# Optimization experiments

Measured on AMD Instinct MI355X. Metric: run time of the kernel, lower is better.

## Reference

```python
import jax, jax.numpy as jnp
import numpy as np

B = 8192      # batch (num nodes)
D = 256       # embedding dim
K = 8         # positives per node -> nnz = B*K
EPS = 1e-8


def setup_inputs() -> dict:
    key = jax.random.key(0)
    k_emb, k_val = jax.random.split(key)
    embeddings = jax.random.normal(k_emb, (B, D), dtype=jnp.float32)
    # structured sparse positive mask: node i is positive with (i+1..i+K) mod B
    # -> unique pairs, row-major sorted (coalesced), no self loops
    rows = jnp.repeat(jnp.arange(B, dtype=jnp.int64), K)           # [B*K]
    offs = jnp.tile(jnp.arange(1, K + 1, dtype=jnp.int64), B)      # [B*K]
    cols = (rows + offs) % B
    pos_vals = jax.random.uniform(k_val, (B * K,), dtype=jnp.float32)
    temperature = jnp.float32(0.5)  # learnable scalar nn.Parameter
    return {
        "embeddings": embeddings,
        "pos_vals": pos_vals,
        "temperature": temperature,
        "pos_row": rows,
        "pos_col": cols,
    }


def reference(embeddings, pos_vals, temperature, pos_row, pos_col):
    n = embeddings.shape[0]
    # F.normalize(p=2, dim=1) with eps=1e-12
    norm = jnp.linalg.norm(embeddings, axis=1, keepdims=True)
    z = embeddings / jnp.maximum(norm, 1e-12)

    temp = jax.nn.softplus(temperature)
    sim = jnp.matmul(z, z.T) / temp                                 # [B,B]
    sim = sim - jax.lax.stop_gradient(jnp.max(sim, axis=1, keepdims=True))

    pos_dense = jnp.zeros((n, n), dtype=bool).at[pos_row, pos_col].set(True)
    identity = jnp.eye(n, dtype=bool)
    neg_mask = (~pos_dense) & (~identity)

    # pos weights: 'inverse_sim' -> 1 - values, min-max normalized
    pos_w = 1.0 - pos_vals
    pos_w = (pos_w - jnp.min(pos_w)) / (jnp.max(pos_w) - jnp.min(pos_w) + EPS)

    # neg weights: 'inverse_sim' -> min-max over negative sims, +1; weight_mat=1 elsewhere
    neg_min = jnp.min(jnp.where(neg_mask, sim, jnp.inf))
    neg_max = jnp.max(jnp.where(neg_mask, sim, -jnp.inf))
    neg_w = (sim - neg_min) / (neg_max - neg_min + EPS) + 1.0
    log_weight = jnp.where(neg_mask, jnp.log(neg_w), 0.0)

    log_probs = sim - jax.nn.logsumexp(sim + log_weight, axis=1, keepdims=True)

    pos_log = log_probs[pos_row, pos_col]   # same ordering as torch boolean index (coalesced mask)
    loss = -jnp.mean(pos_log * pos_w)
    return loss
```

## Files before the change

kernel.cpp:

```cpp
#include <hip/hip_runtime.h>

#define NB 8192
#define ND 256
#define NMASK 8191
#define CEPS 1e-8f
#define L2E 1.4426950408889634f
#define LN2 0.6931471805599453f
#define SC1 0x7F7F7F7F

#if __has_builtin(__builtin_amdgcn_exp2f)
#define EXP2(x) __builtin_amdgcn_exp2f(x)
#else
#define EXP2(x) exp2f(x)
#endif

#define DPPF(x, ctrl) \
  __int_as_float(__builtin_amdgcn_update_dpp(0, __float_as_int(x), (ctrl), 0xF, 0xF, true))

__device__ __forceinline__ float sum16(float x) {
  x += DPPF(x, 0xB1);
  x += DPPF(x, 0x4E);
  x += DPPF(x, 0x124);
  x += DPPF(x, 0x128);
  return x;
}
__device__ __forceinline__ float min16(float x) {
  x = fminf(x, DPPF(x, 0xB1));
  x = fminf(x, DPPF(x, 0x4E));
  x = fminf(x, DPPF(x, 0x124));
  x = fminf(x, DPPF(x, 0x128));
  return x;
}
__device__ __forceinline__ float max16(float x) {
  x = fmaxf(x, DPPF(x, 0xB1));
  x = fmaxf(x, DPPF(x, 0x4E));
  x = fmaxf(x, DPPF(x, 0x124));
  x = fmaxf(x, DPPF(x, 0x128));
  return x;
}

typedef float f32x4 __attribute__((ext_vector_type(4)));
typedef int v8i __attribute__((ext_vector_type(8)));
typedef int v4i __attribute__((ext_vector_type(4)));
union V8 { v8i v; v4i q[2]; };


__global__ void k_norm(const float* __restrict__ emb, const float* __restrict__ temperature,
                       const float* __restrict__ pos_vals, char* __restrict__ zb8,
                       float* __restrict__ bpvmin, float* __restrict__ bpvmax,
                       float* __restrict__ out) {
  const int tid = threadIdx.x, lane = tid & 63, w = tid >> 6;
  const int bid = blockIdx.x;
  if (bid == 0 && tid == 0) out[0] = 0.f;
  float sp = log1pf(expf(temperature[0]));
  float alpha = sqrtf(L2E / sp);
  int row = bid * 4 + w;
  const float4 e = *(const float4*)(emb + row * ND + lane * 4);
  float ss = e.x * e.x + e.y * e.y + e.z * e.z + e.w * e.w;
#pragma unroll
  for (int mk = 1; mk < 64; mk <<= 1) ss += __shfl_xor(ss, mk, 64);
  float rn = alpha / fmaxf(sqrtf(ss), 1e-12f);
  int pk = __builtin_amdgcn_cvt_pk_fp8_f32(e.x * rn, e.y * rn, 0, 0);
  pk = __builtin_amdgcn_cvt_pk_fp8_f32(e.z * rn, e.w * rn, pk, 1);
  *(int*)(zb8 + row * 256 + lane * 4) = pk;
  if (w == 0) {
    float v = (lane < 32) ? pos_vals[bid * 32 + lane] : 0.f;
    float mn = (lane < 32) ? v : INFINITY;
    float mx = (lane < 32) ? v : -INFINITY;
#pragma unroll
    for (int mk = 1; mk < 32; mk <<= 1) {
      mn = fminf(mn, __shfl_xor(mn, mk, 64));
      mx = fmaxf(mx, __shfl_xor(mx, mk, 64));
    }
    if (lane == 0) { bpvmin[bid] = mn; bpvmax[bid] = mx; }
  }
}

__global__ __launch_bounds__(256) void k_gemm(
    const char* __restrict__ zb8, float2* __restrict__ EpR, float2* __restrict__ EpC,
    float* __restrict__ sBand, float* __restrict__ bmin, float* __restrict__ bmax) {
  __shared__ __align__(16) char smem[32768];
  const int tid = threadIdx.x, lane = tid & 63, w = tid >> 6;
  const int l15 = lane & 15, lq = lane >> 4;
  const int bid = blockIdx.x;
  int d, rb;
  if (bid < 2048) { d = bid >> 6; rb = bid & 63; }
  else { d = 32; rb = bid - 2048; }
  const int cb = (rb + d) & 63;
  const int roww = rb * 128 + w * 32;
  const int colbase = cb * 128;

#pragma unroll
  for (int i = 0; i < 8; ++i) {
    int s = w * 8 + i, T = s >> 1, h = s & 1, ct = T >> 1, kc = T & 1;
    const char* g = zb8 + (colbase + ct * 16 + l15) * 256 + kc * 128 + lq * 32 + h * 16;
    __builtin_amdgcn_global_load_lds(
        (const __attribute__((address_space(1))) void*)(g),
        (__attribute__((address_space(3))) void*)(smem + s * 1024), 16, 0, 0);
  }

  V8 aF[2][2];
#pragma unroll
  for (int mt = 0; mt < 2; ++mt) {
    const char* ar = zb8 + (roww + mt * 16 + l15) * 256 + lq * 32;
#pragma unroll
    for (int kc = 0; kc < 2; ++kc) {
      aF[mt][kc].q[0] = *(const v4i*)(ar + kc * 128);
      aF[mt][kc].q[1] = *(const v4i*)(ar + kc * 128 + 16);
    }
  }

  float E1r[8], Ear[8];
#pragma unroll
  for (int i = 0; i < 8; ++i) { E1r[i] = 0.f; Ear[i] = 0.f; }
  float2 cA[4][2];
#pragma unroll
  for (int s = 0; s < 4; ++s) { cA[s][0] = make_float2(0.f, 0.f); cA[s][1] = make_float2(0.f, 0.f); }
  float vmn = INFINITY, vmx = -INFINITY;

  __syncthreads();

#pragma unroll
  for (int step = 0; step < 4; ++step) {
    f32x4 acc[2][2];
#pragma unroll
    for (int mt = 0; mt < 2; ++mt) {
      acc[mt][0] = (f32x4){0.f, 0.f, 0.f, 0.f};
      acc[mt][1] = (f32x4){0.f, 0.f, 0.f, 0.f};
    }
#pragma unroll
    for (int kc = 0; kc < 2; ++kc) {
      V8 b0, b1;
      const char* t0 = smem + ((step * 2 + 0) * 2 + kc) * 2048;
      const char* t1 = smem + ((step * 2 + 1) * 2 + kc) * 2048;
      b0.q[0] = *(const v4i*)(t0 + lane * 16);
      b0.q[1] = *(const v4i*)(t0 + 1024 + lane * 16);
      b1.q[0] = *(const v4i*)(t1 + lane * 16);
      b1.q[1] = *(const v4i*)(t1 + 1024 + lane * 16);
#pragma unroll
      for (int mt = 0; mt < 2; ++mt) {
        acc[mt][0] = __builtin_amdgcn_mfma_scale_f32_16x16x128_f8f6f4(
            aF[mt][kc].v, b0.v, acc[mt][0], 0, 0, 0, SC1, 0, SC1);
        acc[mt][1] = __builtin_amdgcn_mfma_scale_f32_16x16x128_f8f6f4(
            aF[mt][kc].v, b1.v, acc[mt][1], 0, 0, 0, SC1, 0, SC1);
      }
    }
    const int offbase = (colbase + step * 32 + l15) - (roww + lq * 4);
    if (d >= 2) {
#pragma unroll
      for (int mt = 0; mt < 2; ++mt)
#pragma unroll
        for (int nt = 0; nt < 2; ++nt)
#pragma unroll
          for (int reg = 0; reg < 4; ++reg) {
            float t = acc[mt][nt][reg];
            float e = EXP2(t);
            E1r[mt * 4 + reg] += e;
            Ear[mt * 4 + reg] = fmaf(e, t, Ear[mt * 4 + reg]);
            cA[step][nt].x += e;
            cA[step][nt].y = fmaf(e, t, cA[step][nt].y);
            vmn = fminf(vmn, t);
            vmx = fmaxf(vmx, t);
          }
    } else if (d == 1) {
#pragma unroll
      for (int mt = 0; mt < 2; ++mt)
#pragma unroll
        for (int nt = 0; nt < 2; ++nt)
#pragma unroll
          for (int reg = 0; reg < 4; ++reg) {
            float t = acc[mt][nt][reg];
            float e = EXP2(t);
            E1r[mt * 4 + reg] += e;
            Ear[mt * 4 + reg] = fmaf(e, t, Ear[mt * 4 + reg]);
            cA[step][nt].x += e;
            cA[step][nt].y = fmaf(e, t, cA[step][nt].y);
            vmn = fminf(vmn, t);
            vmx = fmaxf(vmx, t);
            int off = (offbase + (nt - mt) * 16 - reg) & NMASK;
            if (off <= 8)
              sBand[(roww + mt * 16 + lq * 4 + reg) * 12 + off] = t;
          }
    } else {
#pragma unroll
      for (int mt = 0; mt < 2; ++mt)
#pragma unroll
        for (int nt = 0; nt < 2; ++nt)
#pragma unroll
          for (int reg = 0; reg < 4; ++reg) {
            float t = acc[mt][nt][reg];
            float e = EXP2(t);
            E1r[mt * 4 + reg] += e;
            Ear[mt * 4 + reg] = fmaf(e, t, Ear[mt * 4 + reg]);
            int off = (offbase + (nt - mt) * 16 - reg) & NMASK;
            bool isB = off <= 8;
            vmn = fminf(vmn, isB ? vmn : t);
            vmx = fmaxf(vmx, isB ? vmx : t);
            if (isB)
              sBand[(roww + mt * 16 + lq * 4 + reg) * 12 + off] = t;
          }
    }
  }

#pragma unroll
  for (int i = 0; i < 8; ++i) {
    E1r[i] = sum16(E1r[i]);
    Ear[i] = sum16(Ear[i]);
  }
  if (l15 == 0) {
#pragma unroll
    for (int mt = 0; mt < 2; ++mt)
#pragma unroll
      for (int reg = 0; reg < 4; ++reg) {
        int row = roww + mt * 16 + lq * 4 + reg;
        EpR[d * NB + row] = make_float2(E1r[mt * 4 + reg], Ear[mt * 4 + reg]);
      }
  }
  vmn = min16(vmn);
  vmx = max16(vmx);
  vmn = fminf(vmn, __shfl_xor(vmn, 16, 64));
  vmx = fmaxf(vmx, __shfl_xor(vmx, 16, 64));
  vmn = fminf(vmn, __shfl_xor(vmn, 32, 64));
  vmx = fmaxf(vmx, __shfl_xor(vmx, 32, 64));
  __syncthreads();
  float2* colAcc = (float2*)smem;
  float* redmm = (float*)(smem + 16384);
  if (d != 0) {
#pragma unroll
    for (int s = 0; s < 4; ++s)
#pragma unroll
      for (int nt = 0; nt < 2; ++nt)
        colAcc[(w * 4 + lq) * 128 + s * 32 + nt * 16 + l15] = cA[s][nt];
  }
  if (lane == 0) { redmm[w] = vmn; redmm[4 + w] = vmx; }
  __syncthreads();
  if (d != 0 && tid < 128) {
    float sx = 0.f, sy = 0.f;
#pragma unroll
    for (int j = 0; j < 16; ++j) {
      float2 p = colAcc[j * 128 + tid];
      sx += p.x;
      sy += p.y;
    }
    EpC[d * NB + colbase + tid] = make_float2(sx, sy);
  }
  if (tid == 0) {
    bmin[bid] = fminf(fminf(redmm[0], redmm[1]), fminf(redmm[2], redmm[3]));
    bmax[bid] = fmaxf(fmaxf(redmm[4], redmm[5]), fmaxf(redmm[6], redmm[7]));
  }
}

__global__ void k_final(const float* __restrict__ pos_vals,
                        const float2* __restrict__ EpR, const float2* __restrict__ EpC,
                        const float* __restrict__ sBand,
                        const float* __restrict__ bmin, const float* __restrict__ bmax,
                        const float* __restrict__ bpvmin, const float* __restrict__ bpvmax,
                        float* __restrict__ out) {
  const int tid = threadIdx.x, lane = tid & 63, w = tid >> 6;
  __shared__ float sv[16];
  __shared__ float coef[4];
  float mn = INFINITY, mx = -INFINITY, pmn = INFINITY, pmx = -INFINITY;
  for (int i = tid; i < 2080; i += 256) { mn = fminf(mn, bmin[i]); mx = fmaxf(mx, bmax[i]); }
  for (int i = tid; i < 2048; i += 256) { pmn = fminf(pmn, bpvmin[i]); pmx = fmaxf(pmx, bpvmax[i]); }
#pragma unroll
  for (int mk = 1; mk < 64; mk <<= 1) {
    mn = fminf(mn, __shfl_xor(mn, mk, 64));
    mx = fmaxf(mx, __shfl_xor(mx, mk, 64));
    pmn = fminf(pmn, __shfl_xor(pmn, mk, 64));
    pmx = fmaxf(pmx, __shfl_xor(pmx, mk, 64));
  }
  if (lane == 0) { sv[w] = mn; sv[4 + w] = mx; sv[8 + w] = pmn; sv[12 + w] = pmx; }
  __syncthreads();
  if (tid == 0) {
    float tmin = fminf(fminf(sv[0], sv[1]), fminf(sv[2], sv[3]));
    float tmax = fmaxf(fmaxf(sv[4], sv[5]), fmaxf(sv[6], sv[7]));
    float pvmin = fminf(fminf(sv[8], sv[9]), fminf(sv[10], sv[11]));
    float pvmax = fmaxf(fmaxf(sv[12], sv[13]), fmaxf(sv[14], sv[15]));
    float At = LN2 / ((tmax - tmin) * LN2 + CEPS);
    coef[0] = At;
    coef[1] = 1.f - At * tmin;
    coef[2] = pvmax;
    coef[3] = 1.f / (pvmax - pvmin + CEPS);
  }
  __syncthreads();
  const float At = coef[0], Bt = coef[1], pvmax = coef[2], pwInv = coef[3];

  int row = blockIdx.x * 256 + tid;
  float e1 = 0.f, ea = 0.f;
#pragma unroll
  for (int dd = 0; dd < 32; ++dd) { float2 p = EpR[dd * NB + row]; e1 += p.x; ea += p.y; }
#pragma unroll
  for (int dd = 1; dd < 32; ++dd) { float2 p = EpC[dd * NB + row]; e1 += p.x; ea += p.y; }
  {
    float2 p = (row < 4096) ? EpR[32 * NB + row] : EpC[32 * NB + row];
    e1 += p.x; ea += p.y;
  }
  float tb[9], Sb = 0.f, Sbt = 0.f;
#pragma unroll
  for (int o = 0; o <= 8; ++o) {
    tb[o] = sBand[row * 12 + o];
    float e = EXP2(tb[o]);
    Sb += e;
    Sbt = fmaf(e, tb[o], Sbt);
  }
  float denom = At * (ea - Sbt) + Bt * (e1 - Sb) + Sb;
  float lse = logf(denom);
  float contrib = 0.f;
#pragma unroll
  for (int k = 0; k < 8; ++k) {
    float v = pos_vals[row * 8 + k];
    contrib += (pvmax - v) * pwInv * (tb[k + 1] * LN2 - lse);
  }
#pragma unroll
  for (int mk = 1; mk < 64; mk <<= 1) contrib += __shfl_xor(contrib, mk, 64);
  __syncthreads();
  if (lane == 0) sv[w] = contrib;
  __syncthreads();
  if (tid == 0)
    atomicAdd(out, -(sv[0] + sv[1] + sv[2] + sv[3]) * (1.0f / 65536.0f));
}

extern "C" void kernel_launch(void* const* d_in, const int* in_sizes, int n_in,
                              void* d_out, int out_size, void* d_ws, size_t ws_size,
                              hipStream_t stream) {
  const float* emb = (const float*)d_in[0];
  const float* pos_vals = (const float*)d_in[1];
  const float* temperature = (const float*)d_in[2];
  float* out = (float*)d_out;

  char* ws = (char*)d_ws;
  size_t off = 0;
  float2* EpR = (float2*)(ws + off); off += (size_t)33 * NB * 8;
  float2* EpC = (float2*)(ws + off); off += (size_t)33 * NB * 8;
  float* sBand = (float*)(ws + off); off += (size_t)NB * 12 * 4;
  float* bmin = (float*)(ws + off); off += 2080 * 4 + 128;
  float* bmax = (float*)(ws + off); off += 2080 * 4 + 128;
  float* bpvmin = (float*)(ws + off); off += 2048 * 4;
  float* bpvmax = (float*)(ws + off); off += 2048 * 4;
  char* zb8 = (char*)(ws + off); off += (size_t)NB * 256;

  k_norm<<<2048, 256, 0, stream>>>(emb, temperature, pos_vals, zb8, bpvmin, bpvmax, out);
  k_gemm<<<2080, 256, 0, stream>>>(zb8, EpR, EpC, sBand, bmin, bmax);
  k_final<<<32, 256, 0, stream>>>(pos_vals, EpR, EpC, sBand, bmin, bmax, bpvmin, bpvmax, out);
}
```

Before: 100.4 us.

## Store per-row partial exp sums row-major and vectorize final reduction

Replaces the two strided partial-sum arrays (indexed by diagonal then row) with a single row-major array of 66 float2 slots per row. The final kernel can then read each row's partials with contiguous float4 loads, and it runs with 64 blocks of 128 threads instead of 32 of 256. The band-storage stride goes from 12 to 16 so band values and pos_vals load as float4, and the d>=2 epilogue uses packed float2 math. In exchange, the GEMM kernel's partial-sum writes become scattered across rows, and extra zero-fill writes are added to pad unused slots.

```diff
diff --git a/kernel.cpp b/kernel.cpp
--- a/kernel.cpp
+++ b/kernel.cpp
@@ -7,6 +7,7 @@
 #define L2E 1.4426950408889634f
 #define LN2 0.6931471805599453f
 #define SC1 0x7F7F7F7F
+#define EPS_T 66
 
 #if __has_builtin(__builtin_amdgcn_exp2f)
 #define EXP2(x) __builtin_amdgcn_exp2f(x)
@@ -40,6 +41,7 @@
 }
 
 typedef float f32x4 __attribute__((ext_vector_type(4)));
+typedef float f32x2 __attribute__((ext_vector_type(2)));
 typedef int v8i __attribute__((ext_vector_type(8)));
 typedef int v4i __attribute__((ext_vector_type(4)));
 union V8 { v8i v; v4i q[2]; };
@@ -47,6 +49,7 @@
 
 __global__ void k_norm(const float* __restrict__ emb, const float* __restrict__ temperature,
                        const float* __restrict__ pos_vals, char* __restrict__ zb8,
+                       float2* __restrict__ Ep,
                        float* __restrict__ bpvmin, float* __restrict__ bpvmax,
                        float* __restrict__ out) {
   const int tid = threadIdx.x, lane = tid & 63, w = tid >> 6;
@@ -63,6 +66,8 @@
   int pk = __builtin_amdgcn_cvt_pk_fp8_f32(e.x * rn, e.y * rn, 0, 0);
   pk = __builtin_amdgcn_cvt_pk_fp8_f32(e.z * rn, e.w * rn, pk, 1);
   *(int*)(zb8 + row * 256 + lane * 4) = pk;
+  if (lane == 0)
+    Ep[(size_t)row * EPS_T + 65] = make_float2(0.f, 0.f);
   if (w == 0) {
     float v = (lane < 32) ? pos_vals[bid * 32 + lane] : 0.f;
     float mn = (lane < 32) ? v : INFINITY;
@@ -77,7 +82,7 @@
 }
 
 __global__ __launch_bounds__(256) void k_gemm(
-    const char* __restrict__ zb8, float2* __restrict__ EpR, float2* __restrict__ EpC,
+    const char* __restrict__ zb8, float2* __restrict__ Ep,
     float* __restrict__ sBand, float* __restrict__ bmin, float* __restrict__ bmax) {
   __shared__ __align__(16) char smem[32768];
   const int tid = threadIdx.x, lane = tid & 63, w = tid >> 6;
@@ -110,9 +115,9 @@
     }
   }
 
-  float E1r[8], Ear[8];
-#pragma unroll
-  for (int i = 0; i < 8; ++i) { E1r[i] = 0.f; Ear[i] = 0.f; }
+  f32x2 E1v[4], Eav[4];
+#pragma unroll
+  for (int i = 0; i < 4; ++i) { E1v[i] = (f32x2){0.f, 0.f}; Eav[i] = (f32x2){0.f, 0.f}; }
   float2 cA[4][2];
 #pragma unroll
   for (int s = 0; s < 4; ++s) { cA[s][0] = make_float2(0.f, 0.f); cA[s][1] = make_float2(0.f, 0.f); }
@@ -150,36 +155,41 @@
 #pragma unroll
       for (int mt = 0; mt < 2; ++mt)
 #pragma unroll
+        for (int nt = 0; nt < 2; ++nt) {
+          f32x2 t01, t23, e01, e23;
+          t01.x = acc[mt][nt][0]; t01.y = acc[mt][nt][1];
+          t23.x = acc[mt][nt][2]; t23.y = acc[mt][nt][3];
+          e01.x = EXP2(t01.x); e01.y = EXP2(t01.y);
+          e23.x = EXP2(t23.x); e23.y = EXP2(t23.y);
+          f32x2 m01 = e01 * t01, m23 = e23 * t23;
+          E1v[mt * 2 + 0] += e01; E1v[mt * 2 + 1] += e23;
+          Eav[mt * 2 + 0] += m01; Eav[mt * 2 + 1] += m23;
+          f32x2 es = e01 + e23, ms = m01 + m23;
+          cA[step][nt].x += es.x + es.y;
+          cA[step][nt].y += ms.x + ms.y;
+          vmn = fminf(fminf(t01.x, t01.y), vmn);
+          vmn = fminf(fminf(t23.x, t23.y), vmn);
+          vmx = fmaxf(fmaxf(t01.x, t01.y), vmx);
+          vmx = fmaxf(fmaxf(t23.x, t23.y), vmx);
+        }
+    } else if (d == 1) {
+#pragma unroll
+      for (int mt = 0; mt < 2; ++mt)
+#pragma unroll
         for (int nt = 0; nt < 2; ++nt)
 #pragma unroll
           for (int reg = 0; reg < 4; ++reg) {
             float t = acc[mt][nt][reg];
             float e = EXP2(t);
-            E1r[mt * 4 + reg] += e;
-            Ear[mt * 4 + reg] = fmaf(e, t, Ear[mt * 4 + reg]);
-            cA[step][nt].x += e;
-            cA[step][nt].y = fmaf(e, t, cA[step][nt].y);
-            vmn = fminf(vmn, t);
-            vmx = fmaxf(vmx, t);
-          }
-    } else if (d == 1) {
-#pragma unroll
-      for (int mt = 0; mt < 2; ++mt)
-#pragma unroll
-        for (int nt = 0; nt < 2; ++nt)
-#pragma unroll
-          for (int reg = 0; reg < 4; ++reg) {
-            float t = acc[mt][nt][reg];
-            float e = EXP2(t);
-            E1r[mt * 4 + reg] += e;
-            Ear[mt * 4 + reg] = fmaf(e, t, Ear[mt * 4 + reg]);
+            E1v[mt * 2 + (reg >> 1)][reg & 1] += e;
+            Eav[mt * 2 + (reg >> 1)][reg & 1] = fmaf(e, t, Eav[mt * 2 + (reg >> 1)][reg & 1]);
             cA[step][nt].x += e;
             cA[step][nt].y = fmaf(e, t, cA[step][nt].y);
             vmn = fminf(vmn, t);
             vmx = fmaxf(vmx, t);
             int off = (offbase + (nt - mt) * 16 - reg) & NMASK;
             if (off <= 8)
-              sBand[(roww + mt * 16 + lq * 4 + reg) * 12 + off] = t;
+              sBand[(roww + mt * 16 + lq * 4 + reg) * 16 + off] = t;
           }
     } else {
 #pragma unroll
@@ -190,30 +200,31 @@
           for (int reg = 0; reg < 4; ++reg) {
             float t = acc[mt][nt][reg];
             float e = EXP2(t);
-            E1r[mt * 4 + reg] += e;
-            Ear[mt * 4 + reg] = fmaf(e, t, Ear[mt * 4 + reg]);
+            E1v[mt * 2 + (reg >> 1)][reg & 1] += e;
+            Eav[mt * 2 + (reg >> 1)][reg & 1] = fmaf(e, t, Eav[mt * 2 + (reg >> 1)][reg & 1]);
             int off = (offbase + (nt - mt) * 16 - reg) & NMASK;
             bool isB = off <= 8;
             vmn = fminf(vmn, isB ? vmn : t);
             vmx = fmaxf(vmx, isB ? vmx : t);
             if (isB)
-              sBand[(roww + mt * 16 + lq * 4 + reg) * 12 + off] = t;
+              sBand[(roww + mt * 16 + lq * 4 + reg) * 16 + off] = t;
           }
     }
   }
 
 #pragma unroll
-  for (int i = 0; i < 8; ++i) {
-    E1r[i] = sum16(E1r[i]);
-    Ear[i] = sum16(Ear[i]);
+  for (int i = 0; i < 4; ++i) {
+    E1v[i].x = sum16(E1v[i].x); E1v[i].y = sum16(E1v[i].y);
+    Eav[i].x = sum16(Eav[i].x); Eav[i].y = sum16(Eav[i].y);
   }
   if (l15 == 0) {
 #pragma unroll
     for (int mt = 0; mt < 2; ++mt)
 #pragma unroll
-      for (int reg = 0; reg < 4; ++reg) {
-        int row = roww + mt * 16 + lq * 4 + reg;
-        EpR[d * NB + row] = make_float2(E1r[mt * 4 + reg], Ear[mt * 4 + reg]);
+      for (int p = 0; p < 2; ++p) {
+        int row = roww + mt * 16 + lq * 4 + p * 2;
+        Ep[(size_t)row * EPS_T + d] = make_float2(E1v[mt * 2 + p].x, Eav[mt * 2 + p].x);
+        Ep[(size_t)(row + 1) * EPS_T + d] = make_float2(E1v[mt * 2 + p].y, Eav[mt * 2 + p].y);
       }
   }
   vmn = min16(vmn);
@@ -242,7 +253,11 @@
       sx += p.x;
       sy += p.y;
     }
-    EpC[d * NB + colbase + tid] = make_float2(sx, sy);
+    Ep[(size_t)(colbase + tid) * EPS_T + 32 + d] = make_float2(sx, sy);
+    if (d == 32) {
+      Ep[(size_t)(rb * 128 + tid) * EPS_T + 64] = make_float2(0.f, 0.f);
+      Ep[(size_t)(colbase + tid) * EPS_T + 32] = make_float2(0.f, 0.f);
+    }
   }
   if (tid == 0) {
     bmin[bid] = fminf(fminf(redmm[0], redmm[1]), fminf(redmm[2], redmm[3]));
@@ -250,18 +265,18 @@
   }
 }
 
-__global__ void k_final(const float* __restrict__ pos_vals,
-                        const float2* __restrict__ EpR, const float2* __restrict__ EpC,
-                        const float* __restrict__ sBand,
-                        const float* __restrict__ bmin, const float* __restrict__ bmax,
-                        const float* __restrict__ bpvmin, const float* __restrict__ bpvmax,
-                        float* __restrict__ out) {
+__global__ __launch_bounds__(128) void k_final(
+    const float* __restrict__ pos_vals, const float2* __restrict__ Ep,
+    const float* __restrict__ sBand,
+    const float* __restrict__ bmin, const float* __restrict__ bmax,
+    const float* __restrict__ bpvmin, const float* __restrict__ bpvmax,
+    float* __restrict__ out) {
   const int tid = threadIdx.x, lane = tid & 63, w = tid >> 6;
-  __shared__ float sv[16];
+  __shared__ float sv[8];
   __shared__ float coef[4];
   float mn = INFINITY, mx = -INFINITY, pmn = INFINITY, pmx = -INFINITY;
-  for (int i = tid; i < 2080; i += 256) { mn = fminf(mn, bmin[i]); mx = fmaxf(mx, bmax[i]); }
-  for (int i = tid; i < 2048; i += 256) { pmn = fminf(pmn, bpvmin[i]); pmx = fmaxf(pmx, bpvmax[i]); }
+  for (int i = tid; i < 2080; i += 128) { mn = fminf(mn, bmin[i]); mx = fmaxf(mx, bmax[i]); }
+  for (int i = tid; i < 2048; i += 128) { pmn = fminf(pmn, bpvmin[i]); pmx = fmaxf(pmx, bpvmax[i]); }
 #pragma unroll
   for (int mk = 1; mk < 64; mk <<= 1) {
     mn = fminf(mn, __shfl_xor(mn, mk, 64));
@@ -269,13 +284,13 @@
     pmn = fminf(pmn, __shfl_xor(pmn, mk, 64));
     pmx = fmaxf(pmx, __shfl_xor(pmx, mk, 64));
   }
-  if (lane == 0) { sv[w] = mn; sv[4 + w] = mx; sv[8 + w] = pmn; sv[12 + w] = pmx; }
+  if (lane == 0) { sv[w] = mn; sv[2 + w] = mx; sv[4 + w] = pmn; sv[6 + w] = pmx; }
   __syncthreads();
   if (tid == 0) {
-    float tmin = fminf(fminf(sv[0], sv[1]), fminf(sv[2], sv[3]));
-    float tmax = fmaxf(fmaxf(sv[4], sv[5]), fmaxf(sv[6], sv[7]));
-    float pvmin = fminf(fminf(sv[8], sv[9]), fminf(sv[10], sv[11]));
-    float pvmax = fmaxf(fmaxf(sv[12], sv[13]), fmaxf(sv[14], sv[15]));
+    float tmin = fminf(sv[0], sv[1]);
+    float tmax = fmaxf(sv[2], sv[3]);
+    float pvmin = fminf(sv[4], sv[5]);
+    float pvmax = fmaxf(sv[6], sv[7]);
     float At = LN2 / ((tmax - tmin) * LN2 + CEPS);
     coef[0] = At;
     coef[1] = 1.f - At * tmin;
@@ -285,39 +300,41 @@
   __syncthreads();
   const float At = coef[0], Bt = coef[1], pvmax = coef[2], pwInv = coef[3];
 
-  int row = blockIdx.x * 256 + tid;
+  const int row = blockIdx.x * 128 + tid;
+  const float4* ep4 = (const float4*)(Ep + (size_t)row * EPS_T);
   float e1 = 0.f, ea = 0.f;
 #pragma unroll
-  for (int dd = 0; dd < 32; ++dd) { float2 p = EpR[dd * NB + row]; e1 += p.x; ea += p.y; }
-#pragma unroll
-  for (int dd = 1; dd < 32; ++dd) { float2 p = EpC[dd * NB + row]; e1 += p.x; ea += p.y; }
-  {
-    float2 p = (row < 4096) ? EpR[32 * NB + row] : EpC[32 * NB + row];
-    e1 += p.x; ea += p.y;
-  }
-  float tb[9], Sb = 0.f, Sbt = 0.f;
+  for (int i = 0; i < 33; ++i) {
+    float4 p = ep4[i];
+    e1 += p.x + p.z;
+    ea += p.y + p.w;
+  }
+  const float4* sb4 = (const float4*)(sBand + (size_t)row * 16);
+  float4 b0 = sb4[0], b1 = sb4[1], b2 = sb4[2];
+  float tb[9] = {b0.x, b0.y, b0.z, b0.w, b1.x, b1.y, b1.z, b1.w, b2.x};
+  float Sb = 0.f, Sbt = 0.f;
 #pragma unroll
   for (int o = 0; o <= 8; ++o) {
-    tb[o] = sBand[row * 12 + o];
     float e = EXP2(tb[o]);
     Sb += e;
     Sbt = fmaf(e, tb[o], Sbt);
   }
   float denom = At * (ea - Sbt) + Bt * (e1 - Sb) + Sb;
   float lse = logf(denom);
+  const float4* pv4 = (const float4*)(pos_vals + (size_t)row * 8);
+  float4 pva = pv4[0], pvb = pv4[1];
+  float pv[8] = {pva.x, pva.y, pva.z, pva.w, pvb.x, pvb.y, pvb.z, pvb.w};
   float contrib = 0.f;
 #pragma unroll
-  for (int k = 0; k < 8; ++k) {
-    float v = pos_vals[row * 8 + k];
-    contrib += (pvmax - v) * pwInv * (tb[k + 1] * LN2 - lse);
-  }
+  for (int k = 0; k < 8; ++k)
+    contrib += (pvmax - pv[k]) * pwInv * (tb[k + 1] * LN2 - lse);
 #pragma unroll
   for (int mk = 1; mk < 64; mk <<= 1) contrib += __shfl_xor(contrib, mk, 64);
   __syncthreads();
   if (lane == 0) sv[w] = contrib;
   __syncthreads();
   if (tid == 0)
-    atomicAdd(out, -(sv[0] + sv[1] + sv[2] + sv[3]) * (1.0f / 65536.0f));
+    atomicAdd(out, -(sv[0] + sv[1]) * (1.0f / 65536.0f));
 }
 
 extern "C" void kernel_launch(void* const* d_in, const int* in_sizes, int n_in,
@@ -330,16 +347,15 @@
 
   char* ws = (char*)d_ws;
   size_t off = 0;
-  float2* EpR = (float2*)(ws + off); off += (size_t)33 * NB * 8;
-  float2* EpC = (float2*)(ws + off); off += (size_t)33 * NB * 8;
-  float* sBand = (float*)(ws + off); off += (size_t)NB * 12 * 4;
+  float2* Ep = (float2*)(ws + off); off += (size_t)NB * EPS_T * 8;
+  float* sBand = (float*)(ws + off); off += (size_t)NB * 16 * 4;
   float* bmin = (float*)(ws + off); off += 2080 * 4 + 128;
   float* bmax = (float*)(ws + off); off += 2080 * 4 + 128;
   float* bpvmin = (float*)(ws + off); off += 2048 * 4;
   float* bpvmax = (float*)(ws + off); off += 2048 * 4;
   char* zb8 = (char*)(ws + off); off += (size_t)NB * 256;
 
-  k_norm<<<2048, 256, 0, stream>>>(emb, temperature, pos_vals, zb8, bpvmin, bpvmax, out);
-  k_gemm<<<2080, 256, 0, stream>>>(zb8, EpR, EpC, sBand, bmin, bmax);
-  k_final<<<32, 256, 0, stream>>>(pos_vals, EpR, EpC, sBand, bmin, bmax, bpvmin, bpvmax, out);
-}
+  k_norm<<<2048, 256, 0, stream>>>(emb, temperature, pos_vals, zb8, Ep, bpvmin, bpvmax, out);
+  k_gemm<<<2080, 256, 0, stream>>>(zb8, Ep, sBand, bmin, bmax);
+  k_final<<<64, 128, 0, stream>>>(pos_vals, Ep, sBand, bmin, bmax, bpvmin, bpvmax, out);
+}
```

Measured after the change: 105.2 us. 4.7% more time.
